# Kernel tuning notes

Hardware: AMD Instinct MI355X
Metric: run time of the kernel (lower is better)

The kernel has to match this reference:

```python
import jax, jax.numpy as jnp
import numpy as np


def setup_inputs() -> dict:
    key = jax.random.key(0)
    ks = jax.random.split(key, 6)
    B, N, S, D, A = 32, 12, 512, 256, 96
    return {
        "value": jax.random.normal(ks[0], (B, N, S, D), dtype=jnp.float32),
        "emb": jax.random.normal(ks[1], (N, S, A), dtype=jnp.float32),
        "Wqk": jax.random.normal(ks[2], (A, D), dtype=jnp.float32) * (A ** -0.5),
        "bqk": jax.random.normal(ks[3], (D,), dtype=jnp.float32) * 0.02,
        "Wv": jax.random.normal(ks[4], (D, D), dtype=jnp.float32) * (D ** -0.5),
        "bv": jax.random.normal(ks[5], (D,), dtype=jnp.float32) * 0.02,
    }


def reference(value, emb, Wqk, bqk, Wv, bv):
    # qk: [n, s, d] -- query and key share the same projection FC_Q_K
    qk = emb @ Wqk + bqk
    v = value @ Wv + bv                      # [b, n, s, d]
    q = jax.nn.softmax(qk, axis=-1)          # softmax over d (last dim of query)
    k = jax.nn.softmax(qk.swapaxes(-1, -2), axis=-1)  # [n, d, s], softmax over s
    # key @ value: [n, d, s] x [b, n, s, e] -> [b, n, d, e] (broadcast over b)
    kv = jnp.einsum('nds,bnse->bnde', k, v)
    # query @ kv: [n, s, d] x [b, n, d, e] -> [b, n, s, e]
    out = jnp.einsum('nsd,bnde->bnse', q, kv)
    return out
```

## Files before the change

kernel.cpp:

```cpp
#include <hip/hip_runtime.h>
#include <hip/hip_bf16.h>

#define B_ 32
#define N_ 12
#define S_ 512
#define D_ 256
#define A_ 96

typedef __attribute__((ext_vector_type(8))) short short8;
typedef __attribute__((ext_vector_type(4))) float float4v;

static __device__ __forceinline__ ushort f2bf(float f) {
  union { float f; unsigned u; } a;
  a.f = f;
  return (ushort)((a.u + 0x7FFFu + ((a.u >> 16) & 1u)) >> 16);
}

__global__ __launch_bounds__(256) void k_qk_softmax_q(
    const float* __restrict__ emb, const float* __restrict__ Wqk,
    const float* __restrict__ bqk, float* __restrict__ qk,
    ushort* __restrict__ qb) {
  int ns = blockIdx.x;
  int d = threadIdx.x;
  __shared__ float se[A_];
  __shared__ float red[8];
  if (d < A_) se[d] = emb[ns * A_ + d];
  __syncthreads();
  float acc = bqk[d];
#pragma unroll
  for (int a = 0; a < A_; ++a) acc = fmaf(se[a], Wqk[a * D_ + d], acc);
  qk[ns * D_ + d] = acc;
  float m = acc;
  for (int off = 32; off; off >>= 1) m = fmaxf(m, __shfl_xor(m, off));
  if ((d & 63) == 0) red[d >> 6] = m;
  __syncthreads();
  m = fmaxf(fmaxf(red[0], red[1]), fmaxf(red[2], red[3]));
  float e = __expf(acc - m);
  float sum = e;
  for (int off = 32; off; off >>= 1) sum += __shfl_xor(sum, off);
  if ((d & 63) == 0) red[4 + (d >> 6)] = sum;
  __syncthreads();
  sum = red[4] + red[5] + red[6] + red[7];
  qb[ns * D_ + d] = f2bf(e / sum);
}

__global__ __launch_bounds__(256) void k_softmax_kT(
    const float* __restrict__ qk, ushort* __restrict__ kTb) {
  int d = blockIdx.x;
  int n = blockIdx.y;
  int s = threadIdx.x;
  __shared__ float red[8];
  float v0 = qk[(n * S_ + s) * D_ + d];
  float v1 = qk[(n * S_ + s + 256) * D_ + d];
  float m = fmaxf(v0, v1);
  for (int off = 32; off; off >>= 1) m = fmaxf(m, __shfl_xor(m, off));
  if ((s & 63) == 0) red[s >> 6] = m;
  __syncthreads();
  m = fmaxf(fmaxf(red[0], red[1]), fmaxf(red[2], red[3]));
  float e0 = __expf(v0 - m), e1 = __expf(v1 - m);
  float sum = e0 + e1;
  for (int off = 32; off; off >>= 1) sum += __shfl_xor(sum, off);
  if ((s & 63) == 0) red[4 + (s >> 6)] = sum;
  __syncthreads();
  sum = red[4] + red[5] + red[6] + red[7];
  float inv = 1.0f / sum;
  kTb[(n * D_ + d) * S_ + s] = f2bf(e0 * inv);
  kTb[(n * D_ + d) * S_ + s + 256] = f2bf(e1 * inv);
}

__global__ __launch_bounds__(256) void k_wvt(const float* __restrict__ Wv,
                                             ushort* __restrict__ WvT) {
  int c = blockIdx.x, e = threadIdx.x;
  WvT[c * D_ + e] = f2bf(Wv[e * D_ + c]);
}

__global__ __launch_bounds__(256) void k_kv0T(
    const ushort* __restrict__ kTb, const float* __restrict__ value,
    ushort* __restrict__ kv0T) {
  const int bx = blockIdx.x;
  const int by = blockIdx.y;
  const int bz = blockIdx.z;
  const int n = bz % N_;
  const int tid = threadIdx.x;
  const int l = tid & 63, w = tid >> 6;
  const int wm = w & 1, wn = w >> 1;
  const int lane16 = l & 15, quad = l >> 4;

  __shared__ ushort ldsA[128 * 72];
  __shared__ ushort ldsB[128 * 72];

  float4v acc[4][4];
#pragma unroll
  for (int i = 0; i < 4; ++i)
#pragma unroll
    for (int j = 0; j < 4; ++j) acc[i][j] = (float4v)0.0f;

  const ushort* kTbase = kTb + ((size_t)(n * D_ + bx * 128)) * S_;
  const float* vbase = value + (size_t)bz * S_ * D_ + by * 128;

  for (int sc = 0; sc < S_; sc += 64) {
    __syncthreads();
#pragma unroll
    for (int it = 0; it < 4; ++it) {
      int id = it * 256 + tid;
      int rd = id >> 3, cc = (id & 7) * 8;
      *(uint4*)(&ldsA[rd * 72 + cc]) =
          *(const uint4*)(kTbase + rd * S_ + sc + cc);
    }
#pragma unroll
    for (int it = 0; it < 16; ++it) {
      int id = it * 256 + tid;
      int e = id & 127, sp = id >> 7;
      float f0 = vbase[(sc + 2 * sp) * D_ + e];
      float f1 = vbase[(sc + 2 * sp + 1) * D_ + e];
      ushort2 p;
      p.x = f2bf(f0);
      p.y = f2bf(f1);
      *(ushort2*)(&ldsB[e * 72 + 2 * sp]) = p;
    }
    __syncthreads();
#pragma unroll
    for (int kc = 0; kc < 64; kc += 32) {
      int ko = kc + quad * 8;
      short8 a[4], b[4];
#pragma unroll
      for (int i = 0; i < 4; ++i)
        a[i] = *(const short8*)(&ldsA[(wm * 64 + i * 16 + lane16) * 72 + ko]);
#pragma unroll
      for (int j = 0; j < 4; ++j)
        b[j] = *(const short8*)(&ldsB[(wn * 64 + j * 16 + lane16) * 72 + ko]);
#pragma unroll
      for (int i = 0; i < 4; ++i)
#pragma unroll
        for (int j = 0; j < 4; ++j)
          acc[i][j] = __builtin_amdgcn_mfma_f32_16x16x32_bf16(a[i], b[j],
                                                              acc[i][j], 0, 0, 0);
    }
  }
  ushort* obase = kv0T + (size_t)bz * D_ * D_;
#pragma unroll
  for (int i = 0; i < 4; ++i) {
#pragma unroll
    for (int j = 0; j < 4; ++j) {
      int e = by * 128 + wn * 64 + j * 16 + lane16;
      int d0 = bx * 128 + wm * 64 + i * 16 + quad * 4;
      ushort4 p;
      p.x = f2bf(acc[i][j][0]);
      p.y = f2bf(acc[i][j][1]);
      p.z = f2bf(acc[i][j][2]);
      p.w = f2bf(acc[i][j][3]);
      *(ushort4*)(obase + e * D_ + d0) = p;
    }
  }
}

__global__ __launch_bounds__(256) void k_out_fused(
    const ushort* __restrict__ qb, const ushort* __restrict__ kv0T,
    const ushort* __restrict__ WvT, const float* __restrict__ bv,
    float* __restrict__ out) {
  const int bx = blockIdx.x;
  const int bz = blockIdx.y;
  const int n = bz % N_;
  const int tid = threadIdx.x;
  const int l = tid & 63, w = tid >> 6;
  const int lane16 = l & 15, quad = l >> 4;

  __shared__ ushort smem[35328];
  ushort* ldsKV = smem;
  ushort* ldsQ = smem + 18432;
  ushort* ldsW = smem;
  ushort* ldsT = smem + 18432;

  const ushort* qbase = qb + ((size_t)n * S_ + bx * 64) * D_;
  const ushort* kvbase = kv0T + (size_t)bz * D_ * D_;

  float4v acc[4][4];
#pragma unroll
  for (int i = 0; i < 4; ++i)
#pragma unroll
    for (int j = 0; j < 4; ++j) acc[i][j] = (float4v)0.0f;

  for (int dc = 0; dc < D_; dc += 64) {
    __syncthreads();
#pragma unroll
    for (int it = 0; it < 2; ++it) {
      int id = it * 256 + tid;
      int r = id >> 3, cc = (id & 7) * 8;
      *(uint4*)(&ldsQ[r * 72 + cc]) = *(const uint4*)(qbase + r * D_ + dc + cc);
    }
#pragma unroll
    for (int it = 0; it < 8; ++it) {
      int id = it * 256 + tid;
      int r = id >> 3, cc = (id & 7) * 8;
      *(uint4*)(&ldsKV[r * 72 + cc]) =
          *(const uint4*)(kvbase + r * D_ + dc + cc);
    }
    __syncthreads();
#pragma unroll
    for (int kc = 0; kc < 64; kc += 32) {
      int ko = kc + quad * 8;
      short8 a[4], b[4];
#pragma unroll
      for (int i = 0; i < 4; ++i)
        a[i] = *(const short8*)(&ldsKV[(w * 64 + i * 16 + lane16) * 72 + ko]);
#pragma unroll
      for (int j = 0; j < 4; ++j)
        b[j] = *(const short8*)(&ldsQ[(j * 16 + lane16) * 72 + ko]);
#pragma unroll
      for (int i = 0; i < 4; ++i)
#pragma unroll
        for (int j = 0; j < 4; ++j)
          acc[i][j] = __builtin_amdgcn_mfma_f32_16x16x32_bf16(a[i], b[j],
                                                              acc[i][j], 0, 0, 0);
    }
  }
  __syncthreads();
#pragma unroll
  for (int i = 0; i < 4; ++i) {
#pragma unroll
    for (int j = 0; j < 4; ++j) {
      int s = j * 16 + lane16;
      int e0 = w * 64 + i * 16 + quad * 4;
      ushort4 p;
      p.x = f2bf(acc[i][j][0]);
      p.y = f2bf(acc[i][j][1]);
      p.z = f2bf(acc[i][j][2]);
      p.w = f2bf(acc[i][j][3]);
      *(ushort4*)(&ldsT[s * 264 + e0]) = p;
    }
  }

  float4v acc2[4][4];
#pragma unroll
  for (int i = 0; i < 4; ++i)
#pragma unroll
    for (int j = 0; j < 4; ++j) acc2[i][j] = (float4v)0.0f;

  for (int ec = 0; ec < D_; ec += 64) {
    __syncthreads();
#pragma unroll
    for (int it = 0; it < 8; ++it) {
      int id = it * 256 + tid;
      int r = id >> 3, cc = (id & 7) * 8;
      *(uint4*)(&ldsW[r * 72 + cc]) = *(const uint4*)(WvT + r * D_ + ec + cc);
    }
    __syncthreads();
#pragma unroll
    for (int kc = 0; kc < 64; kc += 32) {
      int ko = kc + quad * 8;
      short8 a[4], b[4];
#pragma unroll
      for (int i = 0; i < 4; ++i)
        a[i] = *(const short8*)(&ldsT[(i * 16 + lane16) * 264 + ec + ko]);
#pragma unroll
      for (int j = 0; j < 4; ++j)
        b[j] = *(const short8*)(&ldsW[(w * 64 + j * 16 + lane16) * 72 + ko]);
#pragma unroll
      for (int i = 0; i < 4; ++i)
#pragma unroll
        for (int j = 0; j < 4; ++j)
          acc2[i][j] = __builtin_amdgcn_mfma_f32_16x16x32_bf16(a[i], b[j],
                                                               acc2[i][j], 0, 0, 0);
    }
  }
  float* obase = out + (size_t)bz * S_ * D_ + (size_t)bx * 64 * D_;
#pragma unroll
  for (int i = 0; i < 4; ++i) {
#pragma unroll
    for (int j = 0; j < 4; ++j) {
      int s0 = i * 16 + quad * 4;
      int c = w * 64 + j * 16 + lane16;
      float bvc = bv[c];
#pragma unroll
      for (int r = 0; r < 4; ++r)
        obase[(s0 + r) * D_ + c] = acc2[i][j][r] + bvc;
    }
  }
}

extern "C" void kernel_launch(void* const* d_in, const int* in_sizes, int n_in,
                              void* d_out, int out_size, void* d_ws,
                              size_t ws_size, hipStream_t stream) {
  const float* value = (const float*)d_in[0];
  const float* emb   = (const float*)d_in[1];
  const float* Wqk   = (const float*)d_in[2];
  const float* bqk   = (const float*)d_in[3];
  const float* Wv    = (const float*)d_in[4];
  const float* bv    = (const float*)d_in[5];
  float* out = (float*)d_out;

  char* ws = (char*)d_ws;
  float*  qk   = (float*)ws;
  ushort* qb   = (ushort*)(ws + 6291456);
  ushort* kTb  = (ushort*)(ws + 9437184);
  ushort* kv0T = (ushort*)(ws + 12582912);
  ushort* WvT  = (ushort*)(ws + 62914560);

  k_qk_softmax_q<<<dim3(N_ * S_), 256, 0, stream>>>(emb, Wqk, bqk, qk, qb);
  k_softmax_kT<<<dim3(D_, N_), 256, 0, stream>>>(qk, kTb);
  k_wvt<<<dim3(D_), 256, 0, stream>>>(Wv, WvT);
  k_kv0T<<<dim3(2, 2, B_ * N_), 256, 0, stream>>>(kTb, value, kv0T);
  k_out_fused<<<dim3(8, B_ * N_), 256, 0, stream>>>(qb, kv0T, WvT, bv, out);
}
```

Measured before the change: 484.1 us.

## Reassociate Wv projection onto per-head kv matrix instead of output rows

The Wv projection and bias are now applied to the 256x256 kv matrix for each (b,n) in a separate in-place kernel, using the fact that softmax rows of q sum to one so the bias passes through. The previous design multiplied each 512-row output tile by Wv. The final kernel then becomes a plain q @ kvW GEMM. The kv kernel is also retiled so each block covers a 64-wide e slice against all 256 d. This trades one large GEMM for a smaller one at the cost of an extra launch, an extra read/write of kv in bf16, and an added bf16 rounding step on kvW.

```diff
diff --git a/kernel.cpp b/kernel.cpp
--- a/kernel.cpp
+++ b/kernel.cpp
@@ -74,9 +74,169 @@
   WvT[c * D_ + e] = f2bf(Wv[e * D_ + c]);
 }
 
-__global__ __launch_bounds__(256) void k_kv0T(
+__global__ __launch_bounds__(256) void k_kv0(
     const ushort* __restrict__ kTb, const float* __restrict__ value,
-    ushort* __restrict__ kv0T) {
+    ushort* __restrict__ kv0) {
+  const int eb = blockIdx.x * 64;
+  const int bz = blockIdx.y;
+  const int n = bz % N_;
+  const int tid = threadIdx.x;
+  const int l = tid & 63, w = tid >> 6;
+  const int lane16 = l & 15, quad = l >> 4;
+
+  __shared__ ushort ldsV[64 * 72];
+  __shared__ ushort ldsK[256 * 72];
+
+  float4v acc[4][4];
+#pragma unroll
+  for (int i = 0; i < 4; ++i)
+#pragma unroll
+    for (int j = 0; j < 4; ++j) acc[i][j] = (float4v)0.0f;
+
+  const ushort* kTbase = kTb + (size_t)n * D_ * S_;
+  const float* vbase = value + (size_t)bz * S_ * D_ + eb;
+
+  for (int sc = 0; sc < S_; sc += 64) {
+    __syncthreads();
+#pragma unroll
+    for (int it = 0; it < 8; ++it) {
+      int id = it * 256 + tid;
+      int rd = id >> 3, cc = (id & 7) * 8;
+      *(uint4*)(&ldsK[rd * 72 + cc]) =
+          *(const uint4*)(kTbase + rd * S_ + sc + cc);
+    }
+#pragma unroll
+    for (int it = 0; it < 8; ++it) {
+      int id = it * 256 + tid;
+      int e = id & 63, sp = id >> 6;
+      float f0 = vbase[(sc + 2 * sp) * D_ + e];
+      float f1 = vbase[(sc + 2 * sp + 1) * D_ + e];
+      ushort2 p;
+      p.x = f2bf(f0);
+      p.y = f2bf(f1);
+      *(ushort2*)(&ldsV[e * 72 + 2 * sp]) = p;
+    }
+    __syncthreads();
+#pragma unroll
+    for (int kc = 0; kc < 64; kc += 32) {
+      int ko = kc + quad * 8;
+      short8 a[4], b[4];
+#pragma unroll
+      for (int i = 0; i < 4; ++i)
+        a[i] = *(const short8*)(&ldsV[(i * 16 + lane16) * 72 + ko]);
+#pragma unroll
+      for (int j = 0; j < 4; ++j)
+        b[j] = *(const short8*)(&ldsK[(w * 64 + j * 16 + lane16) * 72 + ko]);
+#pragma unroll
+      for (int i = 0; i < 4; ++i)
+#pragma unroll
+        for (int j = 0; j < 4; ++j)
+          acc[i][j] = __builtin_amdgcn_mfma_f32_16x16x32_bf16(a[i], b[j],
+                                                              acc[i][j], 0, 0, 0);
+    }
+  }
+  ushort* obase = kv0 + (size_t)bz * D_ * D_;
+#pragma unroll
+  for (int i = 0; i < 4; ++i) {
+#pragma unroll
+    for (int j = 0; j < 4; ++j) {
+      int d = w * 64 + j * 16 + lane16;
+      int e0 = eb + i * 16 + quad * 4;
+      ushort4 p;
+      p.x = f2bf(acc[i][j][0]);
+      p.y = f2bf(acc[i][j][1]);
+      p.z = f2bf(acc[i][j][2]);
+      p.w = f2bf(acc[i][j][3]);
+      *(ushort4*)(obase + d * D_ + e0) = p;
+    }
+  }
+}
+
+__global__ __launch_bounds__(256) void k_kvw_inplace(
+    ushort* kv0, const ushort* __restrict__ WvT,
+    const float* __restrict__ bv) {
+  const int h = blockIdx.x;
+  const int bz = blockIdx.y;
+  const int tid = threadIdx.x;
+  const int l = tid & 63, w = tid >> 6;
+  const int lane16 = l & 15, quad = l >> 4;
+
+  __shared__ ushort ldsA[128 * 72];
+  __shared__ ushort ldsB[256 * 72];
+
+  float4v acc[2][4][4];
+#pragma unroll
+  for (int m = 0; m < 2; ++m)
+#pragma unroll
+    for (int i = 0; i < 4; ++i)
+#pragma unroll
+      for (int j = 0; j < 4; ++j) acc[m][i][j] = (float4v)0.0f;
+
+  ushort* base = kv0 + (size_t)bz * (D_ * D_) + h * (128 * D_);
+
+  for (int ec = 0; ec < D_; ec += 64) {
+    __syncthreads();
+#pragma unroll
+    for (int it = 0; it < 4; ++it) {
+      int id = it * 256 + tid;
+      int rd = id >> 3, cc = (id & 7) * 8;
+      *(uint4*)(&ldsA[rd * 72 + cc]) =
+          *(const uint4*)(base + rd * D_ + ec + cc);
+    }
+#pragma unroll
+    for (int it = 0; it < 8; ++it) {
+      int id = it * 256 + tid;
+      int rd = id >> 3, cc = (id & 7) * 8;
+      *(uint4*)(&ldsB[rd * 72 + cc]) =
+          *(const uint4*)(WvT + rd * D_ + ec + cc);
+    }
+    __syncthreads();
+#pragma unroll
+    for (int kc = 0; kc < 64; kc += 32) {
+      int ko = kc + quad * 8;
+      short8 a[2][4], b[4];
+#pragma unroll
+      for (int m = 0; m < 2; ++m)
+#pragma unroll
+        for (int i = 0; i < 4; ++i)
+          a[m][i] =
+              *(const short8*)(&ldsA[(m * 64 + i * 16 + lane16) * 72 + ko]);
+#pragma unroll
+      for (int j = 0; j < 4; ++j)
+        b[j] = *(const short8*)(&ldsB[(w * 64 + j * 16 + lane16) * 72 + ko]);
+#pragma unroll
+      for (int m = 0; m < 2; ++m)
+#pragma unroll
+        for (int i = 0; i < 4; ++i)
+#pragma unroll
+          for (int j = 0; j < 4; ++j)
+            acc[m][i][j] = __builtin_amdgcn_mfma_f32_16x16x32_bf16(
+                a[m][i], b[j], acc[m][i][j], 0, 0, 0);
+    }
+  }
+#pragma unroll
+  for (int m = 0; m < 2; ++m) {
+#pragma unroll
+    for (int i = 0; i < 4; ++i) {
+#pragma unroll
+      for (int j = 0; j < 4; ++j) {
+        int c = w * 64 + j * 16 + lane16;
+        int d0 = m * 64 + i * 16 + quad * 4;
+        float bvc = bv[c];
+        ushort4 p;
+        p.x = f2bf(acc[m][i][j][0] + bvc);
+        p.y = f2bf(acc[m][i][j][1] + bvc);
+        p.z = f2bf(acc[m][i][j][2] + bvc);
+        p.w = f2bf(acc[m][i][j][3] + bvc);
+        *(ushort4*)(base + c * 128 + d0) = p;
+      }
+    }
+  }
+}
+
+__global__ __launch_bounds__(256) void k_out(
+    const ushort* __restrict__ qb, const ushort* __restrict__ kvw,
+    float* __restrict__ out) {
   const int bx = blockIdx.x;
   const int by = blockIdx.y;
   const int bz = blockIdx.z;
@@ -95,28 +255,25 @@
 #pragma unroll
     for (int j = 0; j < 4; ++j) acc[i][j] = (float4v)0.0f;
 
-  const ushort* kTbase = kTb + ((size_t)(n * D_ + bx * 128)) * S_;
-  const float* vbase = value + (size_t)bz * S_ * D_ + by * 128;
-
-  for (int sc = 0; sc < S_; sc += 64) {
+  const ushort* abase = qb + (size_t)n * S_ * D_ + bx * 128 * D_;
+  const ushort* bbase = kvw + (size_t)bz * D_ * D_;
+
+  for (int dc = 0; dc < D_; dc += 64) {
     __syncthreads();
 #pragma unroll
     for (int it = 0; it < 4; ++it) {
       int id = it * 256 + tid;
       int rd = id >> 3, cc = (id & 7) * 8;
       *(uint4*)(&ldsA[rd * 72 + cc]) =
-          *(const uint4*)(kTbase + rd * S_ + sc + cc);
-    }
-#pragma unroll
-    for (int it = 0; it < 16; ++it) {
-      int id = it * 256 + tid;
-      int e = id & 127, sp = id >> 7;
-      float f0 = vbase[(sc + 2 * sp) * D_ + e];
-      float f1 = vbase[(sc + 2 * sp + 1) * D_ + e];
-      ushort2 p;
-      p.x = f2bf(f0);
-      p.y = f2bf(f1);
-      *(ushort2*)(&ldsB[e * 72 + 2 * sp]) = p;
+          *(const uint4*)(abase + rd * D_ + dc + cc);
+    }
+#pragma unroll
+    for (int it = 0; it < 4; ++it) {
+      int id = it * 256 + tid;
+      int rd = id >> 3, cc = (id & 7) * 8;
+      *(uint4*)(&ldsB[rd * 72 + cc]) =
+          *(const uint4*)(bbase + (dc >> 7) * 32768 + (by * 128 + rd) * 128 +
+                          (dc & 127) + cc);
     }
     __syncthreads();
 #pragma unroll
@@ -137,143 +294,16 @@
                                                               acc[i][j], 0, 0, 0);
     }
   }
-  ushort* obase = kv0T + (size_t)bz * D_ * D_;
+  float* obase = out + (size_t)bz * S_ * D_;
 #pragma unroll
   for (int i = 0; i < 4; ++i) {
 #pragma unroll
     for (int j = 0; j < 4; ++j) {
-      int e = by * 128 + wn * 64 + j * 16 + lane16;
-      int d0 = bx * 128 + wm * 64 + i * 16 + quad * 4;
-      ushort4 p;
-      p.x = f2bf(acc[i][j][0]);
-      p.y = f2bf(acc[i][j][1]);
-      p.z = f2bf(acc[i][j][2]);
-      p.w = f2bf(acc[i][j][3]);
-      *(ushort4*)(obase + e * D_ + d0) = p;
-    }
-  }
-}
-
-__global__ __launch_bounds__(256) void k_out_fused(
-    const ushort* __restrict__ qb, const ushort* __restrict__ kv0T,
-    const ushort* __restrict__ WvT, const float* __restrict__ bv,
-    float* __restrict__ out) {
-  const int bx = blockIdx.x;
-  const int bz = blockIdx.y;
-  const int n = bz % N_;
-  const int tid = threadIdx.x;
-  const int l = tid & 63, w = tid >> 6;
-  const int lane16 = l & 15, quad = l >> 4;
-
-  __shared__ ushort smem[35328];
-  ushort* ldsKV = smem;
-  ushort* ldsQ = smem + 18432;
-  ushort* ldsW = smem;
-  ushort* ldsT = smem + 18432;
-
-  const ushort* qbase = qb + ((size_t)n * S_ + bx * 64) * D_;
-  const ushort* kvbase = kv0T + (size_t)bz * D_ * D_;
-
-  float4v acc[4][4];
-#pragma unroll
-  for (int i = 0; i < 4; ++i)
-#pragma unroll
-    for (int j = 0; j < 4; ++j) acc[i][j] = (float4v)0.0f;
-
-  for (int dc = 0; dc < D_; dc += 64) {
-    __syncthreads();
-#pragma unroll
-    for (int it = 0; it < 2; ++it) {
-      int id = it * 256 + tid;
-      int r = id >> 3, cc = (id & 7) * 8;
-      *(uint4*)(&ldsQ[r * 72 + cc]) = *(const uint4*)(qbase + r * D_ + dc + cc);
-    }
-#pragma unroll
-    for (int it = 0; it < 8; ++it) {
-      int id = it * 256 + tid;
-      int r = id >> 3, cc = (id & 7) * 8;
-      *(uint4*)(&ldsKV[r * 72 + cc]) =
-          *(const uint4*)(kvbase + r * D_ + dc + cc);
-    }
-    __syncthreads();
-#pragma unroll
-    for (int kc = 0; kc < 64; kc += 32) {
-      int ko = kc + quad * 8;
-      short8 a[4], b[4];
-#pragma unroll
-      for (int i = 0; i < 4; ++i)
-        a[i] = *(const short8*)(&ldsKV[(w * 64 + i * 16 + lane16) * 72 + ko]);
-#pragma unroll
-      for (int j = 0; j < 4; ++j)
-        b[j] = *(const short8*)(&ldsQ[(j * 16 + lane16) * 72 + ko]);
-#pragma unroll
-      for (int i = 0; i < 4; ++i)
-#pragma unroll
-        for (int j = 0; j < 4; ++j)
-          acc[i][j] = __builtin_amdgcn_mfma_f32_16x16x32_bf16(a[i], b[j],
-                                                              acc[i][j], 0, 0, 0);
-    }
-  }
-  __syncthreads();
-#pragma unroll
-  for (int i = 0; i < 4; ++i) {
-#pragma unroll
-    for (int j = 0; j < 4; ++j) {
-      int s = j * 16 + lane16;
-      int e0 = w * 64 + i * 16 + quad * 4;
-      ushort4 p;
-      p.x = f2bf(acc[i][j][0]);
-      p.y = f2bf(acc[i][j][1]);
-      p.z = f2bf(acc[i][j][2]);
-      p.w = f2bf(acc[i][j][3]);
-      *(ushort4*)(&ldsT[s * 264 + e0]) = p;
-    }
-  }
-
-  float4v acc2[4][4];
-#pragma unroll
-  for (int i = 0; i < 4; ++i)
-#pragma unroll
-    for (int j = 0; j < 4; ++j) acc2[i][j] = (float4v)0.0f;
-
-  for (int ec = 0; ec < D_; ec += 64) {
-    __syncthreads();
-#pragma unroll
-    for (int it = 0; it < 8; ++it) {
-      int id = it * 256 + tid;
-      int r = id >> 3, cc = (id & 7) * 8;
-      *(uint4*)(&ldsW[r * 72 + cc]) = *(const uint4*)(WvT + r * D_ + ec + cc);
-    }
-    __syncthreads();
-#pragma unroll
-    for (int kc = 0; kc < 64; kc += 32) {
-      int ko = kc + quad * 8;
-      short8 a[4], b[4];
-#pragma unroll
-      for (int i = 0; i < 4; ++i)
-        a[i] = *(const short8*)(&ldsT[(i * 16 + lane16) * 264 + ec + ko]);
-#pragma unroll
-      for (int j = 0; j < 4; ++j)
-        b[j] = *(const short8*)(&ldsW[(w * 64 + j * 16 + lane16) * 72 + ko]);
-#pragma unroll
-      for (int i = 0; i < 4; ++i)
-#pragma unroll
-        for (int j = 0; j < 4; ++j)
-          acc2[i][j] = __builtin_amdgcn_mfma_f32_16x16x32_bf16(a[i], b[j],
-                                                               acc2[i][j], 0, 0, 0);
-    }
-  }
-  float* obase = out + (size_t)bz * S_ * D_ + (size_t)bx * 64 * D_;
-#pragma unroll
-  for (int i = 0; i < 4; ++i) {
-#pragma unroll
-    for (int j = 0; j < 4; ++j) {
-      int s0 = i * 16 + quad * 4;
-      int c = w * 64 + j * 16 + lane16;
-      float bvc = bv[c];
+      int s0 = bx * 128 + wm * 64 + i * 16 + quad * 4;
+      int c = by * 128 + wn * 64 + j * 16 + lane16;
 #pragma unroll
       for (int r = 0; r < 4; ++r)
-        obase[(s0 + r) * D_ + c] = acc2[i][j][r] + bvc;
+        obase[(s0 + r) * D_ + c] = acc[i][j][r];
     }
   }
 }
@@ -290,15 +320,16 @@
   float* out = (float*)d_out;
 
   char* ws = (char*)d_ws;
-  float*  qk   = (float*)ws;
-  ushort* qb   = (ushort*)(ws + 6291456);
-  ushort* kTb  = (ushort*)(ws + 9437184);
-  ushort* kv0T = (ushort*)(ws + 12582912);
-  ushort* WvT  = (ushort*)(ws + 62914560);
+  float*  qk  = (float*)ws;
+  ushort* qb  = (ushort*)(ws + 6291456);
+  ushort* kTb = (ushort*)(ws + 9437184);
+  ushort* kv0 = (ushort*)(ws + 12582912);
+  ushort* WvT = (ushort*)(ws + 62914560);
 
   k_qk_softmax_q<<<dim3(N_ * S_), 256, 0, stream>>>(emb, Wqk, bqk, qk, qb);
   k_softmax_kT<<<dim3(D_, N_), 256, 0, stream>>>(qk, kTb);
   k_wvt<<<dim3(D_), 256, 0, stream>>>(Wv, WvT);
-  k_kv0T<<<dim3(2, 2, B_ * N_), 256, 0, stream>>>(kTb, value, kv0T);
-  k_out_fused<<<dim3(8, B_ * N_), 256, 0, stream>>>(qb, kv0T, WvT, bv, out);
-}
+  k_kv0<<<dim3(4, B_ * N_), 256, 0, stream>>>(kTb, value, kv0);
+  k_kvw_inplace<<<dim3(2, B_ * N_), 256, 0, stream>>>(kv0, WvT, bv);
+  k_out<<<dim3(4, 2, B_ * N_), 256, 0, stream>>>(qb, kv0, out);
+}
```

Measured after the change: 472.4 us. -2.4%, faster.
